# Kernel optimization log

Hardware: AMD Instinct MI355X
Metric: run time of the kernel (lower is better)

Reference implementation:

```python
import jax, jax.numpy as jnp
import numpy as np

N = 200000   # num_nodes
D = 64       # embedding_dims
B = 4096     # batch of target nodes (batched per-edge processing)
K = 128      # padded in-neighbor count per target
W = 20       # window_size (history deque length)
H = 128      # hidden_size


def setup_inputs() -> dict:
    key = jax.random.key(0)
    ks = jax.random.split(key, 14)
    return {
        "adj_time": jax.random.uniform(ks[0], (N,), jnp.float32),          # last-seen times in [0,1)
        "gc": jax.random.uniform(ks[1], (N,), jnp.float32),                 # per-node centrality scalar (dict_gc)
        "cur_time": jnp.ones((1,), jnp.float32),                            # current event time (>= all stored times)
        "neigh_mask": jnp.ones((B, K), jnp.float32),                        # 1 = valid neighbor slot
        "hist_feat": jax.random.normal(ks[2], (B, W, 2 * D), jnp.float32),  # feature_dict[...]['feature'] deque
        "hist_time": jax.random.uniform(ks[3], (B, W), jnp.float32),        # feature_dict[...]['time'] deque
        "t2v_w": jax.random.normal(ks[4], (D,), jnp.float32),               # Time2Vec('cos') weights
        "t2v_b": jax.random.normal(ks[5], (D,), jnp.float32),
        "node_w": jax.random.normal(ks[6], (D,), jnp.float32),              # linear_node: Linear(1, D)
        "node_b": jax.random.normal(ks[7], (D,), jnp.float32),
        "att_w": jax.random.normal(ks[8], (2 * D,), jnp.float32),           # Attention: score = cat(a,b) @ w + b
        "att_b": jax.random.normal(ks[9], (1,), jnp.float32),
        "weight": jax.random.normal(ks[10], (H, 4 * D), jnp.float32) * 0.05,
        "targets": jax.random.randint(ks[11], (B,), 0, N),
        "neigh_idx": jax.random.randint(ks[12], (B, K), 0, N),
    }


def reference(adj_time, gc, cur_time, neigh_mask, hist_feat, hist_time,
              t2v_w, t2v_b, node_w, node_b, att_w, att_b, weight,
              targets, neigh_idx):
    t = cur_time[0]

    def node_encoding(idx):
        # Time2Vec('cos'): first channel linear, rest cos(w*dt+b)
        dt = jnp.abs(t - adj_time[idx])[..., None]            # [..., 1]
        phase = t2v_w * dt + t2v_b                            # [..., D]
        tv = jnp.concatenate([phase[..., :1], jnp.cos(phase[..., 1:])], axis=-1)
        feat = jax.nn.relu(tv + gc[idx][..., None] * node_w + node_b)
        # F.normalize (L2 over feature dim)
        return feat / jnp.maximum(jnp.linalg.norm(feat, axis=-1, keepdims=True), 1e-12)

    tgt_feat = node_encoding(targets)       # [B, D]
    ngh_feat = node_encoding(neigh_idx)     # [B, K, D]

    # Decayer(2, 'log'): time_score = 1 / (2 * log(e + dt))
    time_score = 1.0 / (2.0 * jnp.log(jnp.e + (t - adj_time[neigh_idx])))   # [B, K]
    # Attention score between target and each neighbor encoding
    att = (tgt_feat @ att_w[:D])[:, None] \
        + jnp.einsum("bkd,d->bk", ngh_feat, att_w[D:]) + att_b[0]           # [B, K]
    score = jax.nn.leaky_relu(time_score + att, 0.01) * neigh_mask          # [B, K]
    neigh_agg = jnp.einsum("bk,bkd->bd", score, ngh_feat)                   # [B, D]

    combined = jnp.concatenate([tgt_feat, neigh_agg], axis=-1)              # [B, 2D]

    # History aggregation with Decayer(2, 'rev'): w = 1 / (2 * (1 + dt))
    hist_w = 1.0 / (2.0 * (1.0 + (t - hist_time)))                          # [B, W]
    hist_agg = jnp.einsum("bw,bwd->bd", hist_w, hist_feat)                  # [B, 2D]

    feat4 = jnp.concatenate([hist_agg, combined], axis=-1)                  # [B, 4D]
    return jax.nn.relu(feat4 @ weight.T)                                    # [B, H]
```

## Files before the change

kernel.cpp:

```cpp
#include <hip/hip_runtime.h>
#include <math.h>

#define NN 200000
#define DD 64
#define BB 4096
#define KK 128
#define WW 20
#define HH 128
#define TPB 512
#define RPB 8

__device__ __forceinline__ float fast_rcp(float x) { return __builtin_amdgcn_rcpf(x); }
__device__ __forceinline__ float fast_rsq(float x) { return __builtin_amdgcn_rsqf(x); }

__global__ __launch_bounds__(512, 4) void fused(
    const float* __restrict__ adj_time, const float* __restrict__ gc,
    const float* __restrict__ cur_time, const float* __restrict__ neigh_mask,
    const float* __restrict__ hist_feat, const float* __restrict__ hist_time,
    const float* __restrict__ t2v_w, const float* __restrict__ t2v_b,
    const float* __restrict__ node_w, const float* __restrict__ node_b,
    const float* __restrict__ att_w, const float* __restrict__ att_b,
    const float* __restrict__ weight,
    const int* __restrict__ targets, const int* __restrict__ neigh_idx,
    float* __restrict__ out)
{
    const int b0   = blockIdx.x * RPB;
    const int tid  = threadIdx.x;
    const int lane = tid & 63;
    const int wv   = tid >> 6;

    __shared__ float2 dtg[RPB * KK];
    __shared__ float  wk[RPB * KK];
    __shared__ float  hws[RPB][WW];
    __shared__ float  stL[RPB];
    __shared__ float  tile[RPB * 256];
    __shared__ float  wl[128 * 33];

    const float t = cur_time[0];

    float ts_r[2], m_r[2];
#pragma unroll
    for (int i = 0; i < 2; ++i) {
        int   slot = tid + i * TPB;
        int   idx  = neigh_idx[b0 * KK + slot];
        m_r[i]     = neigh_mask[b0 * KK + slot];
        float at   = adj_time[idx];
        float g    = gc[idx];
        dtg[slot]  = make_float2(fabsf(t - at), g);
        ts_r[i]    = fast_rcp(2.0f * __logf(2.71828182845904523536f + (t - at)));
    }
    if (tid < RPB * WW) {
        int r = tid / WW, w = tid - r * WW;
        hws[r][w] = fast_rcp(2.0f * (1.0f + (t - hist_time[(b0 + r) * WW + w])));
    }
    {
        int   tg  = targets[b0 + wv];
        float dtT = fabsf(t - adj_time[tg]);
        float gT  = gc[tg];
        float ph  = fmaf(t2v_w[lane], dtT, t2v_b[lane]);
        float tv_ = (lane == 0) ? ph : __cosf(ph);
        float f   = fmaxf(tv_ + fmaf(gT, node_w[lane], node_b[lane]), 0.f);
        float ss  = f * f;
#pragma unroll
        for (int off = 32; off; off >>= 1) ss += __shfl_xor(ss, off, 64);
        float invn = fast_rsq(fmaxf(ss, 1e-24f));
        float tfn  = f * invn;
        float sdt  = tfn * att_w[lane];
#pragma unroll
        for (int off = 32; off; off >>= 1) sdt += __shfl_xor(sdt, off, 64);
        if (lane == 0) stL[wv] = sdt;
        tile[wv * 256 + 128 + lane] = tfn;
    }
    __syncthreads();

    const float ab = att_b[0];
#pragma unroll
    for (int i = 0; i < 2; ++i) {
        int    slot = tid + i * TPB;
        int    r    = slot >> 7;
        float2 dg   = dtg[slot];
        float  s2 = 0.f, sd = 0.f;
#pragma unroll 8
        for (int d = 0; d < 64; ++d) {
            float ph  = fmaf(t2v_w[d], dg.x, t2v_b[d]);
            float cv  = __cosf(ph);
            float tv_ = (d == 0) ? ph : cv;
            float f   = fmaxf(tv_ + fmaf(dg.y, node_w[d], node_b[d]), 0.f);
            s2 = fmaf(f, f, s2);
            sd = fmaf(f, att_w[64 + d], sd);
        }
        float invn = fast_rsq(fmaxf(s2, 1e-24f));
        float sc   = ts_r[i] + stL[r] + sd * invn + ab;
        sc = (sc > 0.f) ? sc : 0.01f * sc;
        wk[slot] = sc * m_r[i] * invn;
    }

#pragma unroll
    for (int i = 0; i < 2; ++i) {
        int col = tid + i * TPB;
        int r = col >> 7, d = col & 127;
        const float* hf = hist_feat + (size_t)(b0 + r) * WW * 128 + d;
        float s = 0.f;
#pragma unroll
        for (int w = 0; w < WW; ++w) s = fmaf(hws[r][w], hf[w * 128], s);
        tile[r * 256 + d] = s;
    }
    __syncthreads();

    {
        float pw = t2v_w[lane], pb = t2v_b[lane];
        float nw = node_w[lane], nb2 = node_b[lane];
        float acc = 0.f;
        const int base = wv * KK;
#pragma unroll 8
        for (int k = 0; k < KK; ++k) {
            float2 dg = dtg[base + k];
            float  w_ = wk[base + k];
            float  ph = fmaf(pw, dg.x, pb);
            float  cv = __cosf(ph);
            float  tv_ = (lane == 0) ? ph : cv;
            float  f  = fmaxf(tv_ + fmaf(dg.y, nw, nb2), 0.f);
            acc = fmaf(w_, f, acc);
        }
        tile[wv * 256 + 192 + lane] = acc;
    }

    const int h = tid & 127;
    const int g = tid >> 7;
    const float* tb = tile + (g * 2) * 256;
    float acc0 = 0.f, acc1 = 0.f;

    for (int c = 0; c < 8; ++c) {
        __syncthreads();
#pragma unroll
        for (int i = 0; i < 8; ++i) {
            int l  = i * TPB + tid;
            int hh = l >> 5, jj = l & 31;
            wl[hh * 33 + jj] = weight[hh * 256 + c * 32 + jj];
        }
        __syncthreads();

#pragma unroll
        for (int jj = 0; jj < 32; jj += 4) {
            float w0 = wl[h * 33 + jj + 0];
            float w1 = wl[h * 33 + jj + 1];
            float w2 = wl[h * 33 + jj + 2];
            float w3 = wl[h * 33 + jj + 3];
            float4 f0 = *(const float4*)(tb + 0 * 256 + c * 32 + jj);
            float4 f1 = *(const float4*)(tb + 1 * 256 + c * 32 + jj);
            acc0 += w0 * f0.x + w1 * f0.y + w2 * f0.z + w3 * f0.w;
            acc1 += w0 * f1.x + w1 * f1.y + w2 * f1.z + w3 * f1.w;
        }
    }

    out[(size_t)(b0 + g * 2 + 0) * 128 + h] = fmaxf(acc0, 0.f);
    out[(size_t)(b0 + g * 2 + 1) * 128 + h] = fmaxf(acc1, 0.f);
}

extern "C" void kernel_launch(void* const* d_in, const int* in_sizes, int n_in,
                              void* d_out, int out_size, void* d_ws, size_t ws_size,
                              hipStream_t stream) {
    const float* adj_time  = (const float*)d_in[0];
    const float* gc        = (const float*)d_in[1];
    const float* cur_time  = (const float*)d_in[2];
    const float* neigh_mask= (const float*)d_in[3];
    const float* hist_feat = (const float*)d_in[4];
    const float* hist_time = (const float*)d_in[5];
    const float* t2v_w     = (const float*)d_in[6];
    const float* t2v_b     = (const float*)d_in[7];
    const float* node_w    = (const float*)d_in[8];
    const float* node_b    = (const float*)d_in[9];
    const float* att_w     = (const float*)d_in[10];
    const float* att_b     = (const float*)d_in[11];
    const float* weight    = (const float*)d_in[12];
    const int*   targets   = (const int*)d_in[13];
    const int*   neigh_idx = (const int*)d_in[14];

    float* out = (float*)d_out;

    fused<<<BB / RPB, TPB, 0, stream>>>(adj_time, gc, cur_time, neigh_mask,
                                        hist_feat, hist_time, t2v_w, t2v_b,
                                        node_w, node_b, att_w, att_b, weight,
                                        targets, neigh_idx, out);
}
```

Baseline: 135.6 us.

## Double block size to 1024 threads and read weight directly in final GEMV

```diff
diff --git a/kernel.cpp b/kernel.cpp
--- a/kernel.cpp
+++ b/kernel.cpp
@@ -7,13 +7,13 @@
 #define KK 128
 #define WW 20
 #define HH 128
-#define TPB 512
+#define TPB 1024
 #define RPB 8
 
 __device__ __forceinline__ float fast_rcp(float x) { return __builtin_amdgcn_rcpf(x); }
 __device__ __forceinline__ float fast_rsq(float x) { return __builtin_amdgcn_rsqf(x); }
 
-__global__ __launch_bounds__(512, 4) void fused(
+__global__ __launch_bounds__(1024, 8) void fused(
     const float* __restrict__ adj_time, const float* __restrict__ gc,
     const float* __restrict__ cur_time, const float* __restrict__ neigh_mask,
     const float* __restrict__ hist_feat, const float* __restrict__ hist_time,
@@ -34,26 +34,25 @@
     __shared__ float  hws[RPB][WW];
     __shared__ float  stL[RPB];
     __shared__ float  tile[RPB * 256];
-    __shared__ float  wl[128 * 33];
+    __shared__ float  aggp[16][64];
 
     const float t = cur_time[0];
 
-    float ts_r[2], m_r[2];
-#pragma unroll
-    for (int i = 0; i < 2; ++i) {
-        int   slot = tid + i * TPB;
+    float ts_k, m_k;
+    {
+        int   slot = tid;
         int   idx  = neigh_idx[b0 * KK + slot];
-        m_r[i]     = neigh_mask[b0 * KK + slot];
+        m_k        = neigh_mask[b0 * KK + slot];
         float at   = adj_time[idx];
         float g    = gc[idx];
         dtg[slot]  = make_float2(fabsf(t - at), g);
-        ts_r[i]    = fast_rcp(2.0f * __logf(2.71828182845904523536f + (t - at)));
+        ts_k       = fast_rcp(2.0f * __logf(2.71828182845904523536f + (t - at)));
     }
     if (tid < RPB * WW) {
         int r = tid / WW, w = tid - r * WW;
         hws[r][w] = fast_rcp(2.0f * (1.0f + (t - hist_time[(b0 + r) * WW + w])));
     }
-    {
+    if (wv < RPB) {
         int   tg  = targets[b0 + wv];
         float dtT = fabsf(t - adj_time[tg]);
         float gT  = gc[tg];
@@ -73,10 +72,9 @@
     }
     __syncthreads();
 
-    const float ab = att_b[0];
-#pragma unroll
-    for (int i = 0; i < 2; ++i) {
-        int    slot = tid + i * TPB;
+    {
+        const float ab = att_b[0];
+        int    slot = tid;
         int    r    = slot >> 7;
         float2 dg   = dtg[slot];
         float  s2 = 0.f, sd = 0.f;
@@ -90,15 +88,13 @@
             sd = fmaf(f, att_w[64 + d], sd);
         }
         float invn = fast_rsq(fmaxf(s2, 1e-24f));
-        float sc   = ts_r[i] + stL[r] + sd * invn + ab;
+        float sc   = ts_k + stL[r] + sd * invn + ab;
         sc = (sc > 0.f) ? sc : 0.01f * sc;
-        wk[slot] = sc * m_r[i] * invn;
+        wk[slot] = sc * m_k * invn;
     }
 
-#pragma unroll
-    for (int i = 0; i < 2; ++i) {
-        int col = tid + i * TPB;
-        int r = col >> 7, d = col & 127;
+    {
+        int r = tid >> 7, d = tid & 127;
         const float* hf = hist_feat + (size_t)(b0 + r) * WW * 128 + d;
         float s = 0.f;
 #pragma unroll
@@ -108,12 +104,14 @@
     __syncthreads();
 
     {
+        const int r   = wv >> 1;
+        const int sub = wv & 1;
         float pw = t2v_w[lane], pb = t2v_b[lane];
         float nw = node_w[lane], nb2 = node_b[lane];
         float acc = 0.f;
-        const int base = wv * KK;
+        const int base = r * KK + sub * 64;
 #pragma unroll 8
-        for (int k = 0; k < KK; ++k) {
+        for (int k = 0; k < 64; ++k) {
             float2 dg = dtg[base + k];
             float  w_ = wk[base + k];
             float  ph = fmaf(pw, dg.x, pb);
@@ -122,39 +120,30 @@
             float  f  = fmaxf(tv_ + fmaf(dg.y, nw, nb2), 0.f);
             acc = fmaf(w_, f, acc);
         }
-        tile[wv * 256 + 192 + lane] = acc;
+        aggp[wv][lane] = acc;
     }
+    __syncthreads();
 
-    const int h = tid & 127;
-    const int g = tid >> 7;
-    const float* tb = tile + (g * 2) * 256;
-    float acc0 = 0.f, acc1 = 0.f;
+    if ((wv & 1) == 0) {
+        int r = wv >> 1;
+        tile[r * 256 + 192 + lane] = aggp[wv][lane] + aggp[wv + 1][lane];
+    }
+    __syncthreads();
 
-    for (int c = 0; c < 8; ++c) {
-        __syncthreads();
-#pragma unroll
-        for (int i = 0; i < 8; ++i) {
-            int l  = i * TPB + tid;
-            int hh = l >> 5, jj = l & 31;
-            wl[hh * 33 + jj] = weight[hh * 256 + c * 32 + jj];
+    {
+        const int h = tid & 127;
+        const int r = tid >> 7;
+        const float4* wrow = (const float4*)(weight + (size_t)h * 256);
+        const float4* tb   = (const float4*)(tile + r * 256);
+        float acc = 0.f;
+#pragma unroll 8
+        for (int j = 0; j < 64; ++j) {
+            float4 w4 = wrow[j];
+            float4 f4 = tb[j];
+            acc += w4.x * f4.x + w4.y * f4.y + w4.z * f4.z + w4.w * f4.w;
         }
-        __syncthreads();
-
-#pragma unroll
-        for (int jj = 0; jj < 32; jj += 4) {
-            float w0 = wl[h * 33 + jj + 0];
-            float w1 = wl[h * 33 + jj + 1];
-            float w2 = wl[h * 33 + jj + 2];
-            float w3 = wl[h * 33 + jj + 3];
-            float4 f0 = *(const float4*)(tb + 0 * 256 + c * 32 + jj);
-            float4 f1 = *(const float4*)(tb + 1 * 256 + c * 32 + jj);
-            acc0 += w0 * f0.x + w1 * f0.y + w2 * f0.z + w3 * f0.w;
-            acc1 += w0 * f1.x + w1 * f1.y + w2 * f1.z + w3 * f1.w;
-        }
+        out[(size_t)(b0 + r) * 128 + h] = fmaxf(acc, 0.f);
     }
-
-    out[(size_t)(b0 + g * 2 + 0) * 128 + h] = fmaxf(acc0, 0.f);
-    out[(size_t)(b0 + g * 2 + 1) * 128 + h] = fmaxf(acc1, 0.f);
 }
 
 extern "C" void kernel_launch(void* const* d_in, const int* in_sizes, int n_in,
```

Result: slower. 176.1 us (+29.8%).
